# Kernel optimization log

Measured on AMD Instinct MI355X. Metric: run time of the kernel, lower is better.

The kernel has to match this reference:

```python
import jax, jax.numpy as jnp
import numpy as np

V, E, U = 32000, 256, 512  # vocab, embed dim, LSTM units
B, S = 16, 130             # batch, seq len


def lstm_layer(x, mask, k, r, b):
    """Keras LSTMCell semantics. x:[B,T,D], mask:[B,T]; gates order i,f,c,o."""
    h0 = jnp.zeros((x.shape[0], U), x.dtype)
    c0 = h0
    xs = jnp.swapaxes(x, 0, 1)      # [T,B,D]
    ms = jnp.swapaxes(mask, 0, 1)   # [T,B]

    def step(carry, inp):
        h, c = carry
        xt, mt = inp
        z = xt @ k + h @ r + b
        i, f, g, o = jnp.split(z, 4, axis=-1)
        i = jax.nn.sigmoid(i); f = jax.nn.sigmoid(f); o = jax.nn.sigmoid(o)
        cn = f * c + i * jnp.tanh(g)
        hn = o * jnp.tanh(cn)
        m = mt[:, None]
        hn = jnp.where(m, hn, h)  # masked steps carry previous state/output
        cn = jnp.where(m, cn, c)
        return (hn, cn), hn

    _, ys = jax.lax.scan(step, (h0, c0), (xs, ms))
    return jnp.swapaxes(ys, 0, 1)  # [B,T,U]


def stacked_lstm(x, mask, params):
    h = x
    for (k, r, b) in params:
        h = lstm_layer(h, mask, k, r, b)
    return h


def setup_inputs() -> dict:
    key = jax.random.key(0)
    ks = jax.random.split(key, 20)
    d = {}
    d["seqs"] = jax.random.randint(ks[0], (B, S), 0, V)
    d["emb"] = jax.random.normal(ks[1], (V, E), jnp.float32) * 0.01
    i = 2
    for pre in ("f", "b"):
        in_dims = [E, U]
        for l in range(2):
            d[f"{pre}k{l}"] = jax.random.normal(ks[i], (in_dims[l], 4 * U), jnp.float32) * 0.05; i += 1
            d[f"{pre}r{l}"] = jax.random.normal(ks[i], (U, 4 * U), jnp.float32) * 0.05; i += 1
            d[f"{pre}b{l}"] = jnp.zeros((4 * U,), jnp.float32)
    d["Wp"] = jax.random.normal(ks[i], (2 * U, V), jnp.float32) * 0.02
    d["bp"] = jnp.zeros((V,), jnp.float32)
    return d


def reference(seqs, emb, fk0, fr0, fb0, fk1, fr1, fb1, bk0, br0, bb0, bk1, br1, bb1, Wp, bp):
    mask = seqs != 0                 # mask_zero=True
    embedded = emb[seqs]             # [B,S,E]
    # forward LM over tokens 0..S-2
    f = stacked_lstm(embedded[:, :-1], mask[:, :-1], [(fk0, fr0, fb0), (fk1, fr1, fb1)])
    # backward LM over tokens 1..S-1 (go_backwards: scan reversed input)
    xb = embedded[:, 1:][:, ::-1]
    mb = mask[:, 1:][:, ::-1]
    b = stacked_lstm(xb, mb, [(bk0, br0, bb0), (bk1, br1, bb1)])
    b_rev = b[:, ::-1]               # tf.reverse -> chronological order
    o = jnp.concatenate([f[:, :-1], b_rev[:, 1:]], axis=-1)  # [B,S-2,2U]
    return o @ Wp + bp               # [B,S-2,V]
```

## Files before the change

kernel.cpp:

```cpp
#include <hip/hip_runtime.h>

typedef __attribute__((ext_vector_type(8))) short bf16x8;
typedef __attribute__((ext_vector_type(4))) float f32x4;

__device__ __forceinline__ unsigned short f2bf(float x){
  union { float f; unsigned u; } v; v.f = x;
  unsigned r = v.u + 0x7FFFu + ((v.u >> 16) & 1u);
  return (unsigned short)(r >> 16);
}

#define BYPASS_ST_SHORT(base, val) \
  asm volatile("global_store_short %0, %1, off sc0 sc1" :: "v"(base), "v"(val))

__device__ __forceinline__ int ld_flag(const int* p){
  int v;
  asm volatile("global_load_dword %0, %1, off sc0 sc1\n\t"
               "s_waitcnt vmcnt(0)"
               : "=v"(v) : "v"(p) : "memory");
  return v;
}

__device__ __forceinline__ void gload_lds16(const void* g, void* l){
  __builtin_amdgcn_global_load_lds(
      (const __attribute__((address_space(1))) unsigned*)g,
      (__attribute__((address_space(3))) unsigned*)l, 16, 0, 0);
}

__global__ void embed_kernel(const int* __restrict__ seqs, const float* __restrict__ emb,
                             unsigned short* __restrict__ x, int* __restrict__ mask,
                             int* __restrict__ flags){
  const int t = blockIdx.x, b = blockIdx.y, l = threadIdx.x;
  if (t == 0 && b == 0){
    #pragma unroll
    for (int j = 0; j < 16; ++j) flags[l + j*64] = 0;
  }
  const int tok = seqs[b*130 + t];
  if (l == 0) mask[b*130 + t] = (tok != 0) ? 1 : 0;
  const float* src = emb + (size_t)tok * 256;
  unsigned short* dst = x + ((size_t)b*130 + t)*256;
  #pragma unroll
  for (int j = 0; j < 4; ++j) dst[l + j*64] = f2bf(src[l + j*64]);
}

__global__ void transpose_bf16(const float* __restrict__ in, unsigned short* __restrict__ out,
                               int R, int C){
  __shared__ float tile[32][33];
  const int c0 = blockIdx.x*32, r0 = blockIdx.y*32;
  const int tx = threadIdx.x, ty = threadIdx.y;
  #pragma unroll
  for (int j = 0; j < 32; j += 8) tile[ty+j][tx] = in[(size_t)(r0+ty+j)*C + (c0+tx)];
  __syncthreads();
  #pragma unroll
  for (int j = 0; j < 32; j += 8) out[(size_t)(c0+ty+j)*R + (r0+tx)] = f2bf(tile[tx][ty+j]);
}

__global__ __launch_bounds__(512, 2) void lstm_coop(
    const unsigned short* __restrict__ x, const int* __restrict__ maskg,
    const unsigned short* __restrict__ fk0T, const unsigned short* __restrict__ fr0T,
    const unsigned short* __restrict__ fk1T, const unsigned short* __restrict__ fr1T,
    const unsigned short* __restrict__ bk0T, const unsigned short* __restrict__ br0T,
    const unsigned short* __restrict__ bk1T, const unsigned short* __restrict__ br1T,
    const float* __restrict__ fb0, const float* __restrict__ fb1,
    const float* __restrict__ bb0, const float* __restrict__ bb1,
    unsigned short* h0f, unsigned short* h0b,
    unsigned short* aproj, int* flags)
{
  const int wg = blockIdx.x;
  const int dir = wg >> 5;
  const int layer = (wg >> 4) & 1;
  const int u0 = (wg & 15) * 32;
  const int tid = threadIdx.x;
  const int w = tid >> 6, l = tid & 63;
  const int gate = w >> 1, half = w & 1;
  const int lr = l & 15, lk = l >> 4;
  const int cglob = gate*512 + u0 + half*16 + lr;

  const unsigned short* kT = (layer == 0) ? (dir ? bk0T : fk0T) : (dir ? bk1T : fk1T);
  const unsigned short* rT = (layer == 0) ? (dir ? br0T : fr0T) : (dir ? br1T : fr1T);
  const float* bias = (layer == 0) ? (dir ? bb0 : fb0) : (dir ? bb1 : fb1);
  unsigned short* h0 = dir ? h0b : h0f;

  int* fown  = flags + (layer*2 + dir)*256;
  int* fprod = flags + dir*256;
  int* fself = fown + (wg & 15)*16;

  bf16x8 wreg[16], kreg[16];
  #pragma unroll
  for (int i = 0; i < 16; ++i)
    wreg[i] = *(const bf16x8*)(rT + (size_t)cglob*512 + i*32 + lk*8);
  if (layer == 0){
    #pragma unroll
    for (int i = 0; i < 8; ++i)
      kreg[i] = *(const bf16x8*)(kT + (size_t)cglob*256 + i*32 + lk*8);
  } else {
    #pragma unroll
    for (int i = 0; i < 16; ++i)
      kreg[i] = *(const bf16x8*)(kT + (size_t)cglob*512 + i*32 + lk*8);
  }

  __shared__ float z_lds[4][16][32];
  __shared__ int mask_s[16*130];
  __shared__ __attribute__((aligned(16))) char h_lds[16*1024];
  __shared__ __attribute__((aligned(16))) char h2_lds[16*1024];
  for (int i = tid; i < 16*130; i += 512) mask_s[i] = maskg[i];

  float c_reg = 0.f, h_reg = 0.f;
  const int gu = tid & 31, gb = tid >> 5;
  const float bzi = bias[u0+gu], bzf = bias[512 + u0+gu];
  const float bzc = bias[1024 + u0+gu], bzo = bias[1536 + u0+gu];
  __syncthreads();

  for (int t = 0; t < 128; ++t){
    if (w == 0){
      const int* fp = nullptr; int tgt = 0;
      if (l < 16){ fp = fown + l*16; tgt = t; }
      else if (l < 32 && layer == 1){ fp = fprod + (l-16)*16; tgt = t + 1; }
      if (fp){
        while (ld_flag(fp) < tgt) __builtin_amdgcn_s_sleep(1);
      }
    }
    __syncthreads();

    const int r0s = w*2;
    if (layer == 0){
      if (t > 0){
        #pragma unroll
        for (int j = 0; j < 2; ++j){
          const int r = r0s + j;
          const unsigned short* g = h0 + ((size_t)(t-1)*16 + r)*512 + ((l ^ (r & 7))*8);
          gload_lds16(g, h_lds + r*1024);
        }
      }
    } else {
      #pragma unroll
      for (int j = 0; j < 2; ++j){
        const int r = r0s + j;
        const unsigned short* g = h0 + ((size_t)t*16 + r)*512 + ((l ^ (r & 7))*8);
        gload_lds16(g, h_lds + r*1024);
      }
      if (t > 0){
        const int prow = dir ? (128 - t) : (t - 1);
        #pragma unroll
        for (int j = 0; j < 2; ++j){
          const int r = r0s + j;
          const unsigned short* g = aproj + ((size_t)(r*128 + prow))*1024 + dir*512 + ((l ^ (r & 7))*8);
          gload_lds16(g, h2_lds + r*1024);
        }
      }
    }

    f32x4 acc = {0.f, 0.f, 0.f, 0.f};
    const int fsw = (lr & 7) << 4;
    if (layer == 0){
      const int pos = dir ? (129 - t) : t;
      const unsigned short* xa = x + ((size_t)lr*130 + pos)*256 + lk*8;
      #pragma unroll
      for (int i = 0; i < 8; ++i){
        bf16x8 a = *(const bf16x8*)(xa + i*32);
        acc = __builtin_amdgcn_mfma_f32_16x16x32_bf16(a, kreg[i], acc, 0, 0, 0);
      }
      if (t > 0){
        asm volatile("s_waitcnt vmcnt(0)" ::: "memory");
        __syncthreads();
        #pragma unroll
        for (int i = 0; i < 16; ++i){
          bf16x8 a = *(const bf16x8*)(h_lds + lr*1024 + ((lk*16 + i*64) ^ fsw));
          acc = __builtin_amdgcn_mfma_f32_16x16x32_bf16(a, wreg[i], acc, 0, 0, 0);
        }
      }
    } else {
      asm volatile("s_waitcnt vmcnt(0)" ::: "memory");
      __syncthreads();
      #pragma unroll
      for (int i = 0; i < 16; ++i){
        bf16x8 a = *(const bf16x8*)(h_lds + lr*1024 + ((lk*16 + i*64) ^ fsw));
        acc = __builtin_amdgcn_mfma_f32_16x16x32_bf16(a, kreg[i], acc, 0, 0, 0);
      }
      if (t > 0){
        #pragma unroll
        for (int i = 0; i < 16; ++i){
          bf16x8 a = *(const bf16x8*)(h2_lds + lr*1024 + ((lk*16 + i*64) ^ fsw));
          acc = __builtin_amdgcn_mfma_f32_16x16x32_bf16(a, wreg[i], acc, 0, 0, 0);
        }
      }
    }
    #pragma unroll
    for (int r = 0; r < 4; ++r) z_lds[gate][lk*4 + r][half*16 + lr] = acc[r];
    __syncthreads();

    {
      const float zi = z_lds[0][gb][gu] + bzi;
      const float zf = z_lds[1][gb][gu] + bzf;
      const float zc = z_lds[2][gb][gu] + bzc;
      const float zo = z_lds[3][gb][gu] + bzo;
      const float iv = 1.f / (1.f + expf(-zi));
      const float fv = 1.f / (1.f + expf(-zf));
      const float ov = 1.f / (1.f + expf(-zo));
      const float gv = tanhf(zc);
      float cn = fv*c_reg + iv*gv;
      float hn = ov*tanhf(cn);
      const int pos = dir ? (129 - t) : t;
      if (mask_s[gb*130 + pos] == 0){ cn = c_reg; hn = h_reg; }
      c_reg = cn; h_reg = hn;
      const unsigned short hb = f2bf(hn);
      if (layer == 0){
        unsigned short* p = h0 + ((size_t)t*16 + gb)*512 + u0 + gu;
        BYPASS_ST_SHORT(p, (unsigned)hb);
      } else {
        const int row = dir ? (127 - t) : t;
        unsigned short* p = aproj + ((size_t)gb*128 + row)*1024 + dir*512 + u0 + gu;
        BYPASS_ST_SHORT(p, (unsigned)hb);
      }
    }
    asm volatile("s_waitcnt vmcnt(0)" ::: "memory");
    __syncthreads();
    if (tid == 0){
      int v = t + 1;
      asm volatile("global_store_dword %0, %1, off sc0 sc1" :: "v"(fself), "v"(v) : "memory");
    }
  }
}

__global__ __launch_bounds__(256) void gemm_bf16(
    const unsigned short* __restrict__ A, const unsigned short* __restrict__ Bt,
    const float* __restrict__ bias, float* __restrict__ C,
    int M, int N, int K)
{
  __shared__ unsigned short lA[128*32], lB[128*32];
  const int tid = threadIdx.x;
  const int w = tid >> 6, l = tid & 63;
  const int wr = w >> 1, wc = w & 1;
  const int lr = l & 15, lk = l >> 4;
  const int brow = blockIdx.y * 128, bcol = blockIdx.x * 128;
  f32x4 acc[4][4] = {};
  for (int k0 = 0; k0 < K; k0 += 32){
    __syncthreads();
    #pragma unroll
    for (int j = 0; j < 2; ++j){
      const int base = w*2048 + j*1024;
      const int L = base + l*16;
      const int Lg = L ^ (((L >> 7) & 3) << 4);
      const int row = Lg >> 6, kb = Lg & 63;
      gload_lds16((const char*)(A + (size_t)(brow+row)*K + k0) + kb, (char*)lA + base);
      gload_lds16((const char*)(Bt + (size_t)(bcol+row)*K + k0) + kb, (char*)lB + base);
    }
    __syncthreads();
    bf16x8 af[4], bfr[4];
    #pragma unroll
    for (int m = 0; m < 4; ++m){
      const int L = (wr*64 + m*16 + lr)*64 + lk*16;
      const int sp = L ^ (((L >> 7) & 3) << 4);
      af[m] = *(const bf16x8*)((char*)lA + sp);
    }
    #pragma unroll
    for (int n = 0; n < 4; ++n){
      const int L = (wc*64 + n*16 + lr)*64 + lk*16;
      const int sp = L ^ (((L >> 7) & 3) << 4);
      bfr[n] = *(const bf16x8*)((char*)lB + sp);
    }
    #pragma unroll
    for (int m = 0; m < 4; ++m)
      #pragma unroll
      for (int n = 0; n < 4; ++n)
        acc[m][n] = __builtin_amdgcn_mfma_f32_16x16x32_bf16(af[m], bfr[n], acc[m][n], 0, 0, 0);
  }
  #pragma unroll
  for (int m = 0; m < 4; ++m){
    #pragma unroll
    for (int n = 0; n < 4; ++n){
      const int col = bcol + wc*64 + n*16 + lr;
      const float bv = bias[col];
      const int row0 = brow + wr*64 + m*16 + lk*4;
      #pragma unroll
      for (int r = 0; r < 4; ++r)
        C[(size_t)(row0 + r)*N + col] = acc[m][n][r] + bv;
    }
  }
}

extern "C" void kernel_launch(void* const* d_in, const int* in_sizes, int n_in,
                              void* d_out, int out_size, void* d_ws, size_t ws_size,
                              hipStream_t stream){
  (void)in_sizes; (void)n_in; (void)out_size; (void)ws_size;
  const int*   seqs = (const int*)d_in[0];
  const float* emb  = (const float*)d_in[1];
  const float* fk0  = (const float*)d_in[2];
  const float* fr0  = (const float*)d_in[3];
  const float* fb0  = (const float*)d_in[4];
  const float* fk1  = (const float*)d_in[5];
  const float* fr1  = (const float*)d_in[6];
  const float* fb1  = (const float*)d_in[7];
  const float* bk0  = (const float*)d_in[8];
  const float* br0  = (const float*)d_in[9];
  const float* bb0  = (const float*)d_in[10];
  const float* bk1  = (const float*)d_in[11];
  const float* br1  = (const float*)d_in[12];
  const float* bb1  = (const float*)d_in[13];
  const float* Wp   = (const float*)d_in[14];
  const float* bp   = (const float*)d_in[15];
  float* out = (float*)d_out;

  char* ws = (char*)d_ws;
  size_t off = 0;
  auto alloc = [&](size_t b){ size_t o = off; off += (b + 255) & ~(size_t)255; return o; };
  int* flags            = (int*)(ws + alloc(4096));
  unsigned short* x     = (unsigned short*)(ws + alloc((size_t)16*130*256*2));
  int* mask             = (int*)(ws + alloc((size_t)16*130*4));
  unsigned short* fk0T  = (unsigned short*)(ws + alloc((size_t)2048*256*2));
  unsigned short* fr0T  = (unsigned short*)(ws + alloc((size_t)2048*512*2));
  unsigned short* fk1T  = (unsigned short*)(ws + alloc((size_t)2048*512*2));
  unsigned short* fr1T  = (unsigned short*)(ws + alloc((size_t)2048*512*2));
  unsigned short* bk0T  = (unsigned short*)(ws + alloc((size_t)2048*256*2));
  unsigned short* br0T  = (unsigned short*)(ws + alloc((size_t)2048*512*2));
  unsigned short* bk1T  = (unsigned short*)(ws + alloc((size_t)2048*512*2));
  unsigned short* br1T  = (unsigned short*)(ws + alloc((size_t)2048*512*2));
  unsigned short* h0f   = (unsigned short*)(ws + alloc((size_t)128*16*512*2));
  unsigned short* h0b   = (unsigned short*)(ws + alloc((size_t)128*16*512*2));
  unsigned short* aproj = (unsigned short*)(ws + alloc((size_t)2048*1024*2));
  unsigned short* WpT   = (unsigned short*)(ws + alloc((size_t)32000*1024*2));

  embed_kernel<<<dim3(130,16), 64, 0, stream>>>(seqs, emb, x, mask, flags);

  dim3 tb(32, 8);
  transpose_bf16<<<dim3(64, 8),   tb, 0, stream>>>(fk0, fk0T, 256, 2048);
  transpose_bf16<<<dim3(64, 16),  tb, 0, stream>>>(fr0, fr0T, 512, 2048);
  transpose_bf16<<<dim3(64, 16),  tb, 0, stream>>>(fk1, fk1T, 512, 2048);
  transpose_bf16<<<dim3(64, 16),  tb, 0, stream>>>(fr1, fr1T, 512, 2048);
  transpose_bf16<<<dim3(64, 8),   tb, 0, stream>>>(bk0, bk0T, 256, 2048);
  transpose_bf16<<<dim3(64, 16),  tb, 0, stream>>>(br0, br0T, 512, 2048);
  transpose_bf16<<<dim3(64, 16),  tb, 0, stream>>>(bk1, bk1T, 512, 2048);
  transpose_bf16<<<dim3(64, 16),  tb, 0, stream>>>(br1, br1T, 512, 2048);
  transpose_bf16<<<dim3(1000, 32), tb, 0, stream>>>(Wp, WpT, 1024, 32000);

  lstm_coop<<<64, 512, 0, stream>>>(x, mask,
      fk0T, fr0T, fk1T, fr1T, bk0T, br0T, bk1T, br1T,
      fb0, fb1, bb0, bb1, h0f, h0b, aproj, flags);

  gemm_bf16<<<dim3(250, 16), 256, 0, stream>>>(aproj, WpT, bp, out, 2048, 32000, 1024);
}
```

Measured before the change: 858.4 us.

## Fold weight transposes into LSTM kernel and overlap Wp transpose with recurrence

Drops the separate transpose launches for the eight LSTM weight matrices. Each LSTM workgroup now reads and converts its slice of fp32 weights straight into registers. The Wp transpose to bf16 moves into 320 extra workgroups of the LSTM launch, so it runs on otherwise idle CUs while the serial recurrence proceeds. The MFMA chains are also split across four independent accumulators to shorten the dependency chain per step. The risks are that extra workgroups could compete for residency with the spin-waiting cooperative blocks, and the strided fp32 weight loads at startup are uncoalesced.

Result: slower. 910.7 us (+6.1%).

```diff
diff --git a/kernel.cpp b/kernel.cpp
--- a/kernel.cpp
+++ b/kernel.cpp
@@ -42,41 +42,56 @@
   for (int j = 0; j < 4; ++j) dst[l + j*64] = f2bf(src[l + j*64]);
 }
 
-__global__ void transpose_bf16(const float* __restrict__ in, unsigned short* __restrict__ out,
-                               int R, int C){
-  __shared__ float tile[32][33];
-  const int c0 = blockIdx.x*32, r0 = blockIdx.y*32;
-  const int tx = threadIdx.x, ty = threadIdx.y;
-  #pragma unroll
-  for (int j = 0; j < 32; j += 8) tile[ty+j][tx] = in[(size_t)(r0+ty+j)*C + (c0+tx)];
-  __syncthreads();
-  #pragma unroll
-  for (int j = 0; j < 32; j += 8) out[(size_t)(c0+ty+j)*R + (r0+tx)] = f2bf(tile[tx][ty+j]);
-}
-
 __global__ __launch_bounds__(512, 2) void lstm_coop(
     const unsigned short* __restrict__ x, const int* __restrict__ maskg,
-    const unsigned short* __restrict__ fk0T, const unsigned short* __restrict__ fr0T,
-    const unsigned short* __restrict__ fk1T, const unsigned short* __restrict__ fr1T,
-    const unsigned short* __restrict__ bk0T, const unsigned short* __restrict__ br0T,
-    const unsigned short* __restrict__ bk1T, const unsigned short* __restrict__ br1T,
+    const float* __restrict__ fk0, const float* __restrict__ fr0,
+    const float* __restrict__ fk1, const float* __restrict__ fr1,
+    const float* __restrict__ bk0, const float* __restrict__ br0,
+    const float* __restrict__ bk1, const float* __restrict__ br1,
     const float* __restrict__ fb0, const float* __restrict__ fb1,
     const float* __restrict__ bb0, const float* __restrict__ bb1,
+    const float* __restrict__ Wp, unsigned short* __restrict__ WpT,
     unsigned short* h0f, unsigned short* h0b,
     unsigned short* aproj, int* flags)
 {
   const int wg = blockIdx.x;
+  const int tid = threadIdx.x;
+
+  __shared__ float z_lds[4][16][32];
+  __shared__ int mask_s[16*130];
+  __shared__ __attribute__((aligned(16))) char h_lds[16*1024];
+  __shared__ __attribute__((aligned(16))) char h2_lds[16*1024];
+
+  if (wg >= 64){
+    float* tf = (float*)h_lds;
+    const int tw = wg - 64;
+    const int tx = tid & 63, ty = tid >> 6;
+    const int orow = tid & 31, oc = tid >> 5;
+    for (int tile = tw; tile < 16000; tile += 320){
+      const int kt = tile / 500, nt = tile - kt*500;
+      const int r0 = kt*32, c0 = nt*64;
+      #pragma unroll
+      for (int j = 0; j < 4; ++j)
+        tf[(ty + 8*j)*65 + tx] = Wp[(size_t)(r0 + ty + 8*j)*32000 + c0 + tx];
+      __syncthreads();
+      #pragma unroll
+      for (int j = 0; j < 4; ++j)
+        WpT[(size_t)(c0 + oc + 16*j)*1024 + r0 + orow] = f2bf(tf[orow*65 + oc + 16*j]);
+      __syncthreads();
+    }
+    return;
+  }
+
   const int dir = wg >> 5;
   const int layer = (wg >> 4) & 1;
   const int u0 = (wg & 15) * 32;
-  const int tid = threadIdx.x;
   const int w = tid >> 6, l = tid & 63;
   const int gate = w >> 1, half = w & 1;
   const int lr = l & 15, lk = l >> 4;
   const int cglob = gate*512 + u0 + half*16 + lr;
 
-  const unsigned short* kT = (layer == 0) ? (dir ? bk0T : fk0T) : (dir ? bk1T : fk1T);
-  const unsigned short* rT = (layer == 0) ? (dir ? br0T : fr0T) : (dir ? br1T : fr1T);
+  const float* kW = (layer == 0) ? (dir ? bk0 : fk0) : (dir ? bk1 : fk1);
+  const float* rW = (layer == 0) ? (dir ? br0 : fr0) : (dir ? br1 : fr1);
   const float* bias = (layer == 0) ? (dir ? bb0 : fb0) : (dir ? bb1 : fb1);
   unsigned short* h0 = dir ? h0b : h0f;
 
@@ -86,22 +101,21 @@
 
   bf16x8 wreg[16], kreg[16];
   #pragma unroll
-  for (int i = 0; i < 16; ++i)
-    wreg[i] = *(const bf16x8*)(rT + (size_t)cglob*512 + i*32 + lk*8);
-  if (layer == 0){
-    #pragma unroll
-    for (int i = 0; i < 8; ++i)
-      kreg[i] = *(const bf16x8*)(kT + (size_t)cglob*256 + i*32 + lk*8);
-  } else {
-    #pragma unroll
-    for (int i = 0; i < 16; ++i)
-      kreg[i] = *(const bf16x8*)(kT + (size_t)cglob*512 + i*32 + lk*8);
-  }
-
-  __shared__ float z_lds[4][16][32];
-  __shared__ int mask_s[16*130];
-  __shared__ __attribute__((aligned(16))) char h_lds[16*1024];
-  __shared__ __attribute__((aligned(16))) char h2_lds[16*1024];
+  for (int i = 0; i < 16; ++i){
+    #pragma unroll
+    for (int j = 0; j < 8; ++j)
+      wreg[i][j] = (short)f2bf(rW[(size_t)(i*32 + lk*8 + j)*2048 + cglob]);
+  }
+  const int nk = (layer == 0) ? 8 : 16;
+  #pragma unroll
+  for (int i = 0; i < 16; ++i){
+    if (i < nk){
+      #pragma unroll
+      for (int j = 0; j < 8; ++j)
+        kreg[i][j] = (short)f2bf(kW[(size_t)(i*32 + lk*8 + j)*2048 + cglob]);
+    }
+  }
+
   for (int i = tid; i < 16*130; i += 512) mask_s[i] = maskg[i];
 
   float c_reg = 0.f, h_reg = 0.f;
@@ -149,43 +163,66 @@
       }
     }
 
-    f32x4 acc = {0.f, 0.f, 0.f, 0.f};
+    f32x4 a0 = {0.f,0.f,0.f,0.f}, a1 = a0, a2 = a0, a3 = a0;
     const int fsw = (lr & 7) << 4;
     if (layer == 0){
       const int pos = dir ? (129 - t) : t;
       const unsigned short* xa = x + ((size_t)lr*130 + pos)*256 + lk*8;
       #pragma unroll
-      for (int i = 0; i < 8; ++i){
-        bf16x8 a = *(const bf16x8*)(xa + i*32);
-        acc = __builtin_amdgcn_mfma_f32_16x16x32_bf16(a, kreg[i], acc, 0, 0, 0);
+      for (int i = 0; i < 8; i += 2){
+        bf16x8 va = *(const bf16x8*)(xa + i*32);
+        bf16x8 vb = *(const bf16x8*)(xa + i*32 + 32);
+        a0 = __builtin_amdgcn_mfma_f32_16x16x32_bf16(va, kreg[i],   a0, 0, 0, 0);
+        a1 = __builtin_amdgcn_mfma_f32_16x16x32_bf16(vb, kreg[i+1], a1, 0, 0, 0);
       }
       if (t > 0){
         asm volatile("s_waitcnt vmcnt(0)" ::: "memory");
         __syncthreads();
         #pragma unroll
-        for (int i = 0; i < 16; ++i){
-          bf16x8 a = *(const bf16x8*)(h_lds + lr*1024 + ((lk*16 + i*64) ^ fsw));
-          acc = __builtin_amdgcn_mfma_f32_16x16x32_bf16(a, wreg[i], acc, 0, 0, 0);
+        for (int i = 0; i < 16; i += 4){
+          bf16x8 v0 = *(const bf16x8*)(h_lds + lr*1024 + ((lk*16 + (i  )*64) ^ fsw));
+          bf16x8 v1 = *(const bf16x8*)(h_lds + lr*1024 + ((lk*16 + (i+1)*64) ^ fsw));
+          bf16x8 v2 = *(const bf16x8*)(h_lds + lr*1024 + ((lk*16 + (i+2)*64) ^ fsw));
+          bf16x8 v3 = *(const bf16x8*)(h_lds + lr*1024 + ((lk*16 + (i+3)*64) ^ fsw));
+          a0 = __builtin_amdgcn_mfma_f32_16x16x32_bf16(v0, wreg[i],   a0, 0, 0, 0);
+          a1 = __builtin_amdgcn_mfma_f32_16x16x32_bf16(v1, wreg[i+1], a1, 0, 0, 0);
+          a2 = __builtin_amdgcn_mfma_f32_16x16x32_bf16(v2, wreg[i+2], a2, 0, 0, 0);
+          a3 = __builtin_amdgcn_mfma_f32_16x16x32_bf16(v3, wreg[i+3], a3, 0, 0, 0);
         }
       }
     } else {
       asm volatile("s_waitcnt vmcnt(0)" ::: "memory");
       __syncthreads();
       #pragma unroll
-      for (int i = 0; i < 16; ++i){
-        bf16x8 a = *(const bf16x8*)(h_lds + lr*1024 + ((lk*16 + i*64) ^ fsw));
-        acc = __builtin_amdgcn_mfma_f32_16x16x32_bf16(a, kreg[i], acc, 0, 0, 0);
+      for (int i = 0; i < 16; i += 4){
+        bf16x8 v0 = *(const bf16x8*)(h_lds + lr*1024 + ((lk*16 + (i  )*64) ^ fsw));
+        bf16x8 v1 = *(const bf16x8*)(h_lds + lr*1024 + ((lk*16 + (i+1)*64) ^ fsw));
+        bf16x8 v2 = *(const bf16x8*)(h_lds + lr*1024 + ((lk*16 + (i+2)*64) ^ fsw));
+        bf16x8 v3 = *(const bf16x8*)(h_lds + lr*1024 + ((lk*16 + (i+3)*64) ^ fsw));
+        a0 = __builtin_amdgcn_mfma_f32_16x16x32_bf16(v0, kreg[i],   a0, 0, 0, 0);
+        a1 = __builtin_amdgcn_mfma_f32_16x16x32_bf16(v1, kreg[i+1], a1, 0, 0, 0);
+        a2 = __builtin_amdgcn_mfma_f32_16x16x32_bf16(v2, kreg[i+2], a2, 0, 0, 0);
+        a3 = __builtin_amdgcn_mfma_f32_16x16x32_bf16(v3, kreg[i+3], a3, 0, 0, 0);
       }
       if (t > 0){
         #pragma unroll
-        for (int i = 0; i < 16; ++i){
-          bf16x8 a = *(const bf16x8*)(h2_lds + lr*1024 + ((lk*16 + i*64) ^ fsw));
-          acc = __builtin_amdgcn_mfma_f32_16x16x32_bf16(a, wreg[i], acc, 0, 0, 0);
+        for (int i = 0; i < 16; i += 4){
+          bf16x8 v0 = *(const bf16x8*)(h2_lds + lr*1024 + ((lk*16 + (i  )*64) ^ fsw));
+          bf16x8 v1 = *(const bf16x8*)(h2_lds + lr*1024 + ((lk*16 + (i+1)*64) ^ fsw));
+          bf16x8 v2 = *(const bf16x8*)(h2_lds + lr*1024 + ((lk*16 + (i+2)*64) ^ fsw));
+          bf16x8 v3 = *(const bf16x8*)(h2_lds + lr*1024 + ((lk*16 + (i+3)*64) ^ fsw));
+          a0 = __builtin_amdgcn_mfma_f32_16x16x32_bf16(v0, wreg[i],   a0, 0, 0, 0);
+          a1 = __builtin_amdgcn_mfma_f32_16x16x32_bf16(v1, wreg[i+1], a1, 0, 0, 0);
+          a2 = __builtin_amdgcn_mfma_f32_16x16x32_bf16(v2, wreg[i+2], a2, 0, 0, 0);
+          a3 = __builtin_amdgcn_mfma_f32_16x16x32_bf16(v3, wreg[i+3], a3, 0, 0, 0);
         }
       }
     }
-    #pragma unroll
-    for (int r = 0; r < 4; ++r) z_lds[gate][lk*4 + r][half*16 + lr] = acc[r];
+    {
+      f32x4 acc = (a0 + a1) + (a2 + a3);
+      #pragma unroll
+      for (int r = 0; r < 4; ++r) z_lds[gate][lk*4 + r][half*16 + lr] = acc[r];
+    }
     __syncthreads();
 
     {
@@ -306,14 +343,6 @@
   int* flags            = (int*)(ws + alloc(4096));
   unsigned short* x     = (unsigned short*)(ws + alloc((size_t)16*130*256*2));
   int* mask             = (int*)(ws + alloc((size_t)16*130*4));
-  unsigned short* fk0T  = (unsigned short*)(ws + alloc((size_t)2048*256*2));
-  unsigned short* fr0T  = (unsigned short*)(ws + alloc((size_t)2048*512*2));
-  unsigned short* fk1T  = (unsigned short*)(ws + alloc((size_t)2048*512*2));
-  unsigned short* fr1T  = (unsigned short*)(ws + alloc((size_t)2048*512*2));
-  unsigned short* bk0T  = (unsigned short*)(ws + alloc((size_t)2048*256*2));
-  unsigned short* br0T  = (unsigned short*)(ws + alloc((size_t)2048*512*2));
-  unsigned short* bk1T  = (unsigned short*)(ws + alloc((size_t)2048*512*2));
-  unsigned short* br1T  = (unsigned short*)(ws + alloc((size_t)2048*512*2));
   unsigned short* h0f   = (unsigned short*)(ws + alloc((size_t)128*16*512*2));
   unsigned short* h0b   = (unsigned short*)(ws + alloc((size_t)128*16*512*2));
   unsigned short* aproj = (unsigned short*)(ws + alloc((size_t)2048*1024*2));
@@ -321,20 +350,9 @@
 
   embed_kernel<<<dim3(130,16), 64, 0, stream>>>(seqs, emb, x, mask, flags);
 
-  dim3 tb(32, 8);
-  transpose_bf16<<<dim3(64, 8),   tb, 0, stream>>>(fk0, fk0T, 256, 2048);
-  transpose_bf16<<<dim3(64, 16),  tb, 0, stream>>>(fr0, fr0T, 512, 2048);
-  transpose_bf16<<<dim3(64, 16),  tb, 0, stream>>>(fk1, fk1T, 512, 2048);
-  transpose_bf16<<<dim3(64, 16),  tb, 0, stream>>>(fr1, fr1T, 512, 2048);
-  transpose_bf16<<<dim3(64, 8),   tb, 0, stream>>>(bk0, bk0T, 256, 2048);
-  transpose_bf16<<<dim3(64, 16),  tb, 0, stream>>>(br0, br0T, 512, 2048);
-  transpose_bf16<<<dim3(64, 16),  tb, 0, stream>>>(bk1, bk1T, 512, 2048);
-  transpose_bf16<<<dim3(64, 16),  tb, 0, stream>>>(br1, br1T, 512, 2048);
-  transpose_bf16<<<dim3(1000, 32), tb, 0, stream>>>(Wp, WpT, 1024, 32000);
-
-  lstm_coop<<<64, 512, 0, stream>>>(x, mask,
-      fk0T, fr0T, fk1T, fr1T, bk0T, br0T, bk1T, br1T,
-      fb0, fb1, bb0, bb1, h0f, h0b, aproj, flags);
+  lstm_coop<<<384, 512, 0, stream>>>(x, mask,
+      fk0, fr0, fk1, fr1, bk0, br0, bk1, br1,
+      fb0, fb1, bb0, bb1, Wp, WpT, h0f, h0b, aproj, flags);
 
   gemm_bf16<<<dim3(250, 16), 256, 0, stream>>>(aproj, WpT, bp, out, 2048, 32000, 1024);
 }
```
